# Kernel optimization log

Hardware: AMD Instinct MI355X
Metric: run time of the kernel (lower is better)

Reference implementation:

```python
import jax, jax.numpy as jnp
import numpy as np

SIZE = 896   # hidden_size
HALF = 448   # hidden_size // 2
BINS = 256   # 2 ** (bits / 2)
B, T = 32, 1024


def _scale(x):
    # [0, BINS-1] ints -> [-1, 1] floats
    return x.astype(jnp.float32) / ((BINS - 1) / 2.0) - 1.0


def _reorder(w):
    # torch GRU layout (r, u, e) each split coarse/fine ->
    # (coarse_r, coarse_u, coarse_e, fine_r, fine_u, fine_e)
    cr, fr, cu, fu, ce, fe = jnp.split(w, 6, axis=0)
    return jnp.concatenate([cr, cu, ce, fr, fu, fe], axis=0)


def setup_inputs():
    key = jax.random.key(0)
    ks = jax.random.split(key, 14)
    s = 0.05
    return {
        'conditional': jax.random.normal(ks[0], (B, 3 * SIZE, T), jnp.float32) * s,
        'w_coarse_in': jax.random.normal(ks[1], (3 * HALF, 2), jnp.float32) * s,
        'w_fine_in': jax.random.normal(ks[2], (3 * HALF, 3), jnp.float32) * s,
        'w_hh': jax.random.normal(ks[3], (3 * SIZE, SIZE), jnp.float32) * s,
        'b_ih': jax.random.normal(ks[4], (3 * SIZE,), jnp.float32) * s,
        'b_hh': jax.random.normal(ks[5], (3 * SIZE,), jnp.float32) * s,
        'wc1': jax.random.normal(ks[6], (HALF, HALF), jnp.float32) * s,
        'bc1': jax.random.normal(ks[7], (HALF,), jnp.float32) * s,
        'wc2': jax.random.normal(ks[8], (BINS, HALF), jnp.float32) * s,
        'bc2': jax.random.normal(ks[9], (BINS,), jnp.float32) * s,
        'wf1': jax.random.normal(ks[10], (HALF, HALF), jnp.float32) * s,
        'bf1': jax.random.normal(ks[11], (HALF,), jnp.float32) * s,
        'wf2': jax.random.normal(ks[12], (BINS, HALF), jnp.float32) * s,
        'bf2': jax.random.normal(ks[13], (BINS,), jnp.float32) * s,
    }


def _gru_softmax_step(hid, ip, hp, W1, b1, W2, b2):
    # hid: [HALF, B]; ip, hp: [3*HALF, B]
    ru = jax.nn.sigmoid(hp[:2 * HALF] + ip[:2 * HALF])
    r, u = ru[:HALF], ru[HALF:]
    e = jnp.tanh(r * hp[2 * HALF:] + ip[2 * HALF:])
    hid = u * hid + (1.0 - u) * e
    h = jax.nn.relu(hid.T @ W1.T + b1)          # [B, HALF]
    logits = h @ W2.T + b2                       # [B, BINS]
    sample = jnp.argmax(logits, axis=1).astype(jnp.int32)  # argmax=True path
    return hid, sample


def reference(conditional, w_coarse_in, w_fine_in, w_hh, b_ih, b_hh,
              wc1, bc1, wc2, bc2, wf1, bf1, wf2, bf2):
    batch, _, sig_len = conditional.shape
    # [B, 3*SIZE, T] -> [B, T, 3, SIZE], add input bias, split coarse/fine halves
    cond = conditional.transpose(0, 2, 1).reshape(batch, sig_len, 3, SIZE)
    g = cond + b_ih.reshape(3, SIZE)
    # reshape keeps gate order (r, u, e) concatenated along last dim
    bias_c = g[..., :HALF].reshape(batch, sig_len, 3 * HALF).transpose(1, 2, 0)  # [T, 3H, B]
    bias_f = g[..., HALF:].reshape(batch, sig_len, 3 * HALF).transpose(1, 2, 0)

    w_hh_r = _reorder(w_hh)                 # [3*SIZE, SIZE]
    b_hh_r = _reorder(b_hh[:, None])        # [3*SIZE, 1]

    def step(carry, xs):
        coarse, fine, c_hid, f_hid = carry
        bc, bf = xs
        hidden = jnp.concatenate([c_hid, f_hid], axis=0)        # [SIZE, B]
        hp = w_hh_r @ hidden + b_hh_r                            # [3*SIZE, B]
        hp_c, hp_f = hp[:3 * HALF], hp[3 * HALF:]
        cin = jnp.stack([_scale(coarse), _scale(fine)], axis=1)  # [B, 2]
        c_hid, new_coarse = _gru_softmax_step(
            c_hid, w_coarse_in @ cin.T + bc, hp_c, wc1, bc1, wc2, bc2)
        fin = jnp.stack([_scale(coarse), _scale(fine), _scale(new_coarse)], axis=1)  # [B, 3]
        f_hid, new_fine = _gru_softmax_step(
            f_hid, w_fine_in @ fin.T + bf, hp_f, wf1, bf1, wf2, bf2)
        return (new_coarse, new_fine, c_hid, f_hid), (new_coarse, new_fine)

    init = (jnp.full((batch,), BINS // 2, jnp.int32),   # go coarse sample
            jnp.zeros((batch,), jnp.int32),              # go fine sample
            jnp.zeros((HALF, batch), jnp.float32),
            jnp.zeros((HALF, batch), jnp.float32))
    carry, (oc, of) = jax.lax.scan(step, init, (bias_c, bias_f))
    final_hidden = jnp.concatenate([carry[2], carry[3]], axis=0)  # [SIZE, B]
    return oc.T, of.T, final_hidden
```

## Files before the change

kernel.cpp:

```cpp
#include <hip/hip_runtime.h>
#include <math.h>


#define HALFN  448
#define SIZEN  896
#define RTOT   2688
#define NB     32
#define TSTEPS 1024
#define NWG    224
#define NTHR   512
#define CONDSTR (RTOT * TSTEPS)

#define OFF_HID0  0
#define OFF_HID1  28672
#define OFF_H1GC  57344
#define OFF_H1GF  71680
#define OFF_NCP   86016
#define OFF_NFP   86080
#define OFF_CTR   86144
#define OFF_FLAGS 86400

typedef unsigned long long u64t;

__device__ __forceinline__ int orig_row(int r) {
  int c = r / HALFN, o = r - c * HALFN;
  int oc = (c < 3) ? (2 * c) : (2 * (c - 3) + 1);
  return oc * HALFN + o;
}
__device__ __forceinline__ float sigm(float x) { return 1.0f / (1.0f + expf(-x)); }

__device__ __forceinline__ float gload(const float* p) {
  return __hip_atomic_load(const_cast<float*>(p), __ATOMIC_RELAXED, __HIP_MEMORY_SCOPE_AGENT);
}
__device__ __forceinline__ void gstore(float* p, float v) {
  __hip_atomic_store(p, v, __ATOMIC_RELAXED, __HIP_MEMORY_SCOPE_AGENT);
}
__device__ __forceinline__ u64t gload64(const u64t* p) {
  return __hip_atomic_load(const_cast<u64t*>(p), __ATOMIC_RELAXED, __HIP_MEMORY_SCOPE_AGENT);
}
__device__ __forceinline__ void gstore64(u64t* p, u64t v) {
  __hip_atomic_store(p, v, __ATOMIC_RELAXED, __HIP_MEMORY_SCOPE_AGENT);
}
__device__ __forceinline__ void gmax64(u64t* p, u64t v) {
  __hip_atomic_fetch_max(p, v, __ATOMIC_RELAXED, __HIP_MEMORY_SCOPE_AGENT);
}
__device__ __forceinline__ unsigned ctrload(const unsigned* p) {
  return __hip_atomic_load(const_cast<unsigned*>(p), __ATOMIC_RELAXED, __HIP_MEMORY_SCOPE_AGENT);
}
__device__ __forceinline__ unsigned f2ord(float f) {
  unsigned u = __float_as_uint(f);
  return (u & 0x80000000u) ? ~u : (u | 0x80000000u);
}

struct __align__(16) SM {
  float whh[12][SIZEN];
  float wc1l[2][HALFN];
  float wf1l[2][HALFN];
  float wc2l[8][HALFN];
  float wf2l[8][HALFN];
  float red[8][12][32];
  float condw[12][16][33];
  float hps[6][32];
  float hpfl[6][32];
  float chid[2][32];
  float fhid[2][32];
  float scvo[32];
  float sfvo[32];
  float sncn[32];
  float logit8[8][32];
  float wcil[2][3][2];
  float wfil[2][3][3];
  float bihl[12];
  float bhh_l[12];
  int   pflag;
};

__device__ __forceinline__ void gridbar(unsigned* flags, unsigned ep, int& dead) {
  asm volatile("s_waitcnt vmcnt(0)" ::: "memory");
  __syncthreads();
  if (threadIdx.x == 0)
    __hip_atomic_store(&flags[blockIdx.x], ep, __ATOMIC_RELAXED, __HIP_MEMORY_SCOPE_AGENT);
  if (!dead) {
    int iters = 0;
    for (;;) {
      int ok = 1;
      if (threadIdx.x < NWG) {
        unsigned v = __hip_atomic_load(&flags[threadIdx.x], __ATOMIC_RELAXED, __HIP_MEMORY_SCOPE_AGENT);
        ok = (v >= ep) ? 1 : 0;
      }
      if (__syncthreads_and(ok)) break;
      if (++iters > (1 << 20)) { dead = 1; break; }
      __builtin_amdgcn_s_sleep(1);
    }
  } else {
    __syncthreads();
  }
}

__device__ __forceinline__ void pollctr(unsigned* ctr, unsigned target, int* pf, int& dead) {
  if (!dead) {
    int it = 0;
    for (;;) {
      if (threadIdx.x == 0) *pf = (ctrload(ctr) >= target) ? 1 : 0;
      __syncthreads();
      int f = *pf;
      __syncthreads();
      if (f) break;
      if (++it > (1 << 20)) { dead = 1; break; }
      __builtin_amdgcn_s_sleep(1);
    }
  } else {
    __syncthreads(); __syncthreads();
  }
}

extern "C" __global__ void wavernn_init(float* ws) {
  int i = blockIdx.x * blockDim.x + threadIdx.x;
  int st = gridDim.x * blockDim.x;
  for (int k = i; k < 2 * SIZEN * NB; k += st) ws[k] = 0.0f;
  if (i < 64) ((u64t*)(ws + OFF_NCP))[i] = 0ull;
  if (i < 2) ((unsigned*)(ws + OFF_CTR))[i] = 0u;
  if (i < 256) ((unsigned*)(ws + OFF_FLAGS))[i] = 0u;
}

extern "C" __global__ void __launch_bounds__(NTHR)
wavernn_persist(const float* __restrict__ cond,
                const float* __restrict__ wci, const float* __restrict__ wfi,
                const float* __restrict__ whh, const float* __restrict__ bih,
                const float* __restrict__ bhh,
                const float* __restrict__ wc1, const float* __restrict__ bc1,
                const float* __restrict__ wc2, const float* __restrict__ bc2,
                const float* __restrict__ wf1, const float* __restrict__ bf1,
                const float* __restrict__ wf2, const float* __restrict__ bf2,
                float* __restrict__ out, float* ws) {
  __shared__ SM sm;

  float* hid0 = ws + OFF_HID0;
  float* hid1 = ws + OFF_HID1;
  float* h1gc = ws + OFF_H1GC;
  float* h1gf = ws + OFF_H1GF;
  u64t*  ncp  = (u64t*)(ws + OFF_NCP);
  u64t*  nfp  = (u64t*)(ws + OFF_NFP);
  unsigned* ctr = (unsigned*)(ws + OFF_CTR);
  unsigned* flags = (unsigned*)(ws + OFF_FLAGS);

  const int w = blockIdx.x, tid = threadIdx.x;
  const int b = tid & 31, ks = tid >> 5;
  const bool isHead = (w < NB);
  unsigned ep = 0;
  int dead = 0;

#pragma unroll
  for (int rr = 0; rr < 12; rr++) {
    int R = (rr >> 1) * HALFN + 2 * w + (rr & 1);
    const float* src = whh + (size_t)orig_row(R) * SIZEN;
    for (int k = tid * 4; k < SIZEN; k += NTHR * 4)
      *(float4*)&sm.whh[rr][k] = *(const float4*)&src[k];
  }
  if (tid < 12) sm.bhh_l[tid] = bhh[orig_row((tid >> 1) * HALFN + 2 * w + (tid & 1))];
  for (int k = tid * 4; k < HALFN; k += NTHR * 4) {
    *(float4*)&sm.wc1l[0][k] = *(const float4*)&wc1[(size_t)(2 * w) * HALFN + k];
    *(float4*)&sm.wc1l[1][k] = *(const float4*)&wc1[(size_t)(2 * w + 1) * HALFN + k];
    *(float4*)&sm.wf1l[0][k] = *(const float4*)&wf1[(size_t)(2 * w) * HALFN + k];
    *(float4*)&sm.wf1l[1][k] = *(const float4*)&wf1[(size_t)(2 * w + 1) * HALFN + k];
  }
  if (isHead) {
#pragma unroll
    for (int rr = 0; rr < 8; rr++) {
      for (int k = tid * 4; k < HALFN; k += NTHR * 4) {
        *(float4*)&sm.wc2l[rr][k] = *(const float4*)&wc2[(size_t)(w * 8 + rr) * HALFN + k];
        *(float4*)&sm.wf2l[rr][k] = *(const float4*)&wf2[(size_t)(w * 8 + rr) * HALFN + k];
      }
    }
  }
  if (tid < 12) {
    int rk = tid;
    int R = ((rk >= 6) ? HALFN : 0) + ((rk % 6) >> 1) * SIZEN + 2 * w + (rk & 1);
    sm.bihl[rk] = bih[R];
  }
  if (tid < 2) {
    int j = 2 * w + tid;
#pragma unroll
    for (int g = 0; g < 3; g++) {
      sm.wcil[tid][g][0] = wci[(g * HALFN + j) * 2 + 0];
      sm.wcil[tid][g][1] = wci[(g * HALFN + j) * 2 + 1];
      sm.wfil[tid][g][0] = wfi[(g * HALFN + j) * 3 + 0];
      sm.wfil[tid][g][1] = wfi[(g * HALFN + j) * 3 + 1];
      sm.wfil[tid][g][2] = wfi[(g * HALFN + j) * 3 + 2];
    }
  }
  if (tid < 64) { sm.chid[tid >> 5][tid & 31] = 0.0f; sm.fhid[tid >> 5][tid & 31] = 0.0f; }
  if (tid < 32) { sm.scvo[tid] = 128.0f * (2.0f / 255.0f) - 1.0f; sm.sfvo[tid] = -1.0f; }
  __syncthreads();

  for (int t = 0; t < TSTEPS; ++t) {
    const float* hprev = (t & 1) ? hid0 : hid1;
    float*       hcur  = (t & 1) ? hid1 : hid0;
    const int tt = t & 15;

    {
      if (tt == 0) {
        for (int idx = tid; idx < 1536; idx += NTHR) {
          int rk = idx >> 7, rem = idx & 127;
          int bb = rem >> 2, part = rem & 3;
          int R = ((rk >= 6) ? HALFN : 0) + ((rk % 6) >> 1) * SIZEN + 2 * w + (rk & 1);
          float4 v = *(const float4*)&cond[(size_t)bb * CONDSTR + (size_t)R * TSTEPS + t + part * 4];
          sm.condw[rk][part * 4 + 0][bb] = v.x;
          sm.condw[rk][part * 4 + 1][bb] = v.y;
          sm.condw[rk][part * 4 + 2][bb] = v.z;
          sm.condw[rk][part * 4 + 3][bb] = v.w;
        }
      }

      float acc[12];
#pragma unroll
      for (int rr = 0; rr < 12; rr++) acc[rr] = 0.0f;
      const int k0 = ks * 56;
      const float* hcol = hprev + b;
#pragma unroll 2
      for (int k = k0; k < k0 + 56; k += 4) {
        float h0 = gload(&hcol[(k + 0) * 32]), h1v = gload(&hcol[(k + 1) * 32]);
        float h2 = gload(&hcol[(k + 2) * 32]), h3  = gload(&hcol[(k + 3) * 32]);
#pragma unroll
        for (int rr = 0; rr < 12; rr++) {
          const float4 wv = *(const float4*)&sm.whh[rr][k];
          acc[rr] = fmaf(wv.x, h0, fmaf(wv.y, h1v, fmaf(wv.z, h2, fmaf(wv.w, h3, acc[rr]))));
        }
      }
#pragma unroll
      for (int rr = 0; rr < 12; rr++) acc[rr] += __shfl_xor(acc[rr], 32);
      __syncthreads();
      if ((tid & 32) == 0) {
        int slot = ks >> 1;
#pragma unroll
        for (int rr = 0; rr < 12; rr++) sm.red[slot][rr][b] = acc[rr];
      }
      __syncthreads();
      if (tid < 384) {
        int rr = tid >> 5, bb = tid & 31;
        float s = sm.bhh_l[rr];
#pragma unroll
        for (int kk = 0; kk < 8; kk++) s += sm.red[kk][rr][bb];
        if (rr < 6) sm.hps[rr][bb] = s;
        else        sm.hpfl[rr - 6][bb] = s;
      }
      if (t > 0) {
        pollctr(&ctr[1], 32u * (unsigned)t, &sm.pflag, dead);
        if (tid < 32) {
          u64t p = gload64(&nfp[tid]);
          unsigned nf = 0xFFFFFFFFu - (unsigned)(p & 0xFFFFFFFFull);
          sm.sfvo[tid] = (float)nf * (2.0f / 255.0f) - 1.0f;
          if (isHead && tid == w) out[32768 + (size_t)w * TSTEPS + (t - 1)] = (float)nf;
        }
      }
      __syncthreads();
      if (tid < 64) {
        int q = tid >> 5, bb = tid & 31;
        float sc = sm.scvo[bb], sf = sm.sfvo[bb];
        float ipr = sm.wcil[q][0][0] * sc + sm.wcil[q][0][1] * sf + sm.condw[0 + q][tt][bb] + sm.bihl[0 + q];
        float ipu = sm.wcil[q][1][0] * sc + sm.wcil[q][1][1] * sf + sm.condw[2 + q][tt][bb] + sm.bihl[2 + q];
        float ipe = sm.wcil[q][2][0] * sc + sm.wcil[q][2][1] * sf + sm.condw[4 + q][tt][bb] + sm.bihl[4 + q];
        float r = sigm(sm.hps[0 + q][bb] + ipr);
        float u = sigm(sm.hps[2 + q][bb] + ipu);
        float e = tanhf(fmaf(r, sm.hps[4 + q][bb], ipe));
        float hnew = u * sm.chid[q][bb] + (1.0f - u) * e;
        sm.chid[q][bb] = hnew;
        gstore(&hcur[(size_t)(2 * w + q) * 32 + bb], hnew);
      }
    }
    gridbar(flags, ++ep, dead);

    {
      const int k0 = ks * 28;
      float a0 = 0.0f, a1 = 0.0f;
      const float* hcc = hcur + b;
#pragma unroll
      for (int k = k0; k < k0 + 28; k += 4) {
        float h0 = gload(&hcc[(k + 0) * 32]), h1v = gload(&hcc[(k + 1) * 32]);
        float h2 = gload(&hcc[(k + 2) * 32]), h3  = gload(&hcc[(k + 3) * 32]);
        float4 v0 = *(const float4*)&sm.wc1l[0][k];
        a0 = fmaf(v0.x, h0, fmaf(v0.y, h1v, fmaf(v0.z, h2, fmaf(v0.w, h3, a0))));
        float4 v1 = *(const float4*)&sm.wc1l[1][k];
        a1 = fmaf(v1.x, h0, fmaf(v1.y, h1v, fmaf(v1.z, h2, fmaf(v1.w, h3, a1))));
      }
      a0 += __shfl_xor(a0, 32); a1 += __shfl_xor(a1, 32);
      __syncthreads();
      if ((tid & 32) == 0) { sm.red[ks >> 1][0][b] = a0; sm.red[ks >> 1][1][b] = a1; }
      if (isHead && tid == 256) gstore64(&ncp[w], 0ull);
      __syncthreads();
      if (tid < 64) {
        int rr = tid >> 5, bb = tid & 31;
        float s = bc1[2 * w + rr];
#pragma unroll
        for (int kk = 0; kk < 8; kk++) s += sm.red[kk][rr][bb];
        gstore(&h1gc[(size_t)(2 * w + rr) * 32 + bb], fmaxf(s, 0.0f));
      }
    }
    gridbar(flags, ++ep, dead);

    if (isHead) {
      const int k0 = ks * 28;
      float acc[8];
#pragma unroll
      for (int rr = 0; rr < 8; rr++) acc[rr] = 0.0f;
      const float* hh = h1gc + b;
#pragma unroll
      for (int k = k0; k < k0 + 28; k += 4) {
        float h0 = gload(&hh[(k + 0) * 32]), h1v = gload(&hh[(k + 1) * 32]);
        float h2 = gload(&hh[(k + 2) * 32]), h3  = gload(&hh[(k + 3) * 32]);
#pragma unroll
        for (int rr = 0; rr < 8; rr++) {
          const float4 wv = *(const float4*)&sm.wc2l[rr][k];
          acc[rr] = fmaf(wv.x, h0, fmaf(wv.y, h1v, fmaf(wv.z, h2, fmaf(wv.w, h3, acc[rr]))));
        }
      }
#pragma unroll
      for (int rr = 0; rr < 8; rr++) acc[rr] += __shfl_xor(acc[rr], 32);
      __syncthreads();
      if ((tid & 32) == 0) {
        int slot = ks >> 1;
#pragma unroll
        for (int rr = 0; rr < 8; rr++) sm.red[slot][rr][b] = acc[rr];
      }
      __syncthreads();
      if (tid < 256) {
        int rr = tid >> 5, bb = tid & 31;
        float s = bc2[w * 8 + rr];
#pragma unroll
        for (int kk = 0; kk < 8; kk++) s += sm.red[kk][rr][bb];
        sm.logit8[rr][bb] = s;
      }
      __syncthreads();
      if (tid < 32) {
        float bv = sm.logit8[0][tid]; int bi = 0;
#pragma unroll
        for (int rr = 1; rr < 8; rr++) {
          float x = sm.logit8[rr][tid];
          if (x > bv) { bv = x; bi = rr; }
        }
        u64t pack = ((u64t)f2ord(bv) << 32) | (u64t)(0xFFFFFFFFu - (unsigned)(w * 8 + bi));
        gmax64(&ncp[tid], pack);
      }
      asm volatile("s_waitcnt vmcnt(0)" ::: "memory");
      __syncthreads();
      if (tid == 0) __hip_atomic_fetch_add(&ctr[0], 1u, __ATOMIC_RELAXED, __HIP_MEMORY_SCOPE_AGENT);
    }
    pollctr(&ctr[0], 32u * (unsigned)(t + 1), &sm.pflag, dead);

    {
      if (tid < 32) {
        u64t p = gload64(&ncp[tid]);
        unsigned nc = 0xFFFFFFFFu - (unsigned)(p & 0xFFFFFFFFull);
        sm.sncn[tid] = (float)nc * (2.0f / 255.0f) - 1.0f;
        if (isHead && tid == w) out[(size_t)w * TSTEPS + t] = (float)nc;
      }
      __syncthreads();
      if (tid < 64) {
        int q = tid >> 5, bb = tid & 31;
        float sc = sm.scvo[bb], sf = sm.sfvo[bb], snc = sm.sncn[bb];
        float ipr = sm.wfil[q][0][0] * sc + sm.wfil[q][0][1] * sf + sm.wfil[q][0][2] * snc
                  + sm.condw[6 + q][tt][bb] + sm.bihl[6 + q];
        float ipu = sm.wfil[q][1][0] * sc + sm.wfil[q][1][1] * sf + sm.wfil[q][1][2] * snc
                  + sm.condw[8 + q][tt][bb] + sm.bihl[8 + q];
        float ipe = sm.wfil[q][2][0] * sc + sm.wfil[q][2][1] * sf + sm.wfil[q][2][2] * snc
                  + sm.condw[10 + q][tt][bb] + sm.bihl[10 + q];
        float r = sigm(sm.hpfl[0 + q][bb] + ipr);
        float u = sigm(sm.hpfl[2 + q][bb] + ipu);
        float e = tanhf(fmaf(r, sm.hpfl[4 + q][bb], ipe));
        float hnew = u * sm.fhid[q][bb] + (1.0f - u) * e;
        sm.fhid[q][bb] = hnew;
        gstore(&hcur[(size_t)(HALFN + 2 * w + q) * 32 + bb], hnew);
      }
      __syncthreads();
      if (tid < 32) sm.scvo[tid] = sm.sncn[tid];
    }
    gridbar(flags, ++ep, dead);

    {
      const int k0 = ks * 28;
      float a0 = 0.0f, a1 = 0.0f;
      const float* hff = hcur + HALFN * 32 + b;
#pragma unroll
      for (int k = k0; k < k0 + 28; k += 4) {
        float h0 = gload(&hff[(k + 0) * 32]), h1v = gload(&hff[(k + 1) * 32]);
        float h2 = gload(&hff[(k + 2) * 32]), h3  = gload(&hff[(k + 3) * 32]);
        float4 v0 = *(const float4*)&sm.wf1l[0][k];
        a0 = fmaf(v0.x, h0, fmaf(v0.y, h1v, fmaf(v0.z, h2, fmaf(v0.w, h3, a0))));
        float4 v1 = *(const float4*)&sm.wf1l[1][k];
        a1 = fmaf(v1.x, h0, fmaf(v1.y, h1v, fmaf(v1.z, h2, fmaf(v1.w, h3, a1))));
      }
      a0 += __shfl_xor(a0, 32); a1 += __shfl_xor(a1, 32);
      __syncthreads();
      if ((tid & 32) == 0) { sm.red[ks >> 1][0][b] = a0; sm.red[ks >> 1][1][b] = a1; }
      if (isHead && tid == 256) gstore64(&nfp[w], 0ull);
      __syncthreads();
      if (tid < 64) {
        int rr = tid >> 5, bb = tid & 31;
        float s = bf1[2 * w + rr];
#pragma unroll
        for (int kk = 0; kk < 8; kk++) s += sm.red[kk][rr][bb];
        gstore(&h1gf[(size_t)(2 * w + rr) * 32 + bb], fmaxf(s, 0.0f));
      }
    }
    gridbar(flags, ++ep, dead);

    if (isHead) {
      const int k0 = ks * 28;
      float acc[8];
#pragma unroll
      for (int rr = 0; rr < 8; rr++) acc[rr] = 0.0f;
      const float* hh = h1gf + b;
#pragma unroll
      for (int k = k0; k < k0 + 28; k += 4) {
        float h0 = gload(&hh[(k + 0) * 32]), h1v = gload(&hh[(k + 1) * 32]);
        float h2 = gload(&hh[(k + 2) * 32]), h3  = gload(&hh[(k + 3) * 32]);
#pragma unroll
        for (int rr = 0; rr < 8; rr++) {
          const float4 wv = *(const float4*)&sm.wf2l[rr][k];
          acc[rr] = fmaf(wv.x, h0, fmaf(wv.y, h1v, fmaf(wv.z, h2, fmaf(wv.w, h3, acc[rr]))));
        }
      }
#pragma unroll
      for (int rr = 0; rr < 8; rr++) acc[rr] += __shfl_xor(acc[rr], 32);
      __syncthreads();
      if ((tid & 32) == 0) {
        int slot = ks >> 1;
#pragma unroll
        for (int rr = 0; rr < 8; rr++) sm.red[slot][rr][b] = acc[rr];
      }
      __syncthreads();
      if (tid < 256) {
        int rr = tid >> 5, bb = tid & 31;
        float s = bf2[w * 8 + rr];
#pragma unroll
        for (int kk = 0; kk < 8; kk++) s += sm.red[kk][rr][bb];
        sm.logit8[rr][bb] = s;
      }
      __syncthreads();
      if (tid < 32) {
        float bv = sm.logit8[0][tid]; int bi = 0;
#pragma unroll
        for (int rr = 1; rr < 8; rr++) {
          float x = sm.logit8[rr][tid];
          if (x > bv) { bv = x; bi = rr; }
        }
        u64t pack = ((u64t)f2ord(bv) << 32) | (u64t)(0xFFFFFFFFu - (unsigned)(w * 8 + bi));
        gmax64(&nfp[tid], pack);
      }
      asm volatile("s_waitcnt vmcnt(0)" ::: "memory");
      __syncthreads();
      if (tid == 0) __hip_atomic_fetch_add(&ctr[1], 1u, __ATOMIC_RELAXED, __HIP_MEMORY_SCOPE_AGENT);
    }
  }

  pollctr(&ctr[1], 32u * (unsigned)TSTEPS, &sm.pflag, dead);
  if (tid < 32 && isHead && tid == w) {
    u64t p = gload64(&nfp[tid]);
    unsigned nf = 0xFFFFFFFFu - (unsigned)(p & 0xFFFFFFFFull);
    out[32768 + (size_t)w * TSTEPS + (TSTEPS - 1)] = (float)nf;
  }
  if (tid < 64) {
    int q = tid >> 5, bb = tid & 31;
    out[65536 + (size_t)(2 * w + q) * 32 + bb]         = sm.chid[q][bb];
    out[65536 + (size_t)(HALFN + 2 * w + q) * 32 + bb] = sm.fhid[q][bb];
  }
}

extern "C" void kernel_launch(void* const* d_in, const int* in_sizes, int n_in,
                              void* d_out, int out_size, void* d_ws, size_t ws_size,
                              hipStream_t stream) {
  const float* cond = (const float*)d_in[0];
  const float* wci  = (const float*)d_in[1];
  const float* wfi  = (const float*)d_in[2];
  const float* whh  = (const float*)d_in[3];
  const float* bih  = (const float*)d_in[4];
  const float* bhh  = (const float*)d_in[5];
  const float* wc1  = (const float*)d_in[6];
  const float* bc1  = (const float*)d_in[7];
  const float* wc2  = (const float*)d_in[8];
  const float* bc2  = (const float*)d_in[9];
  const float* wf1  = (const float*)d_in[10];
  const float* bf1  = (const float*)d_in[11];
  const float* wf2  = (const float*)d_in[12];
  const float* bf2  = (const float*)d_in[13];
  float* out = (float*)d_out;
  float* ws  = (float*)d_ws;

  hipLaunchKernelGGL(wavernn_init, dim3(64), dim3(256), 0, stream, ws);
  hipLaunchKernelGGL(wavernn_persist, dim3(NWG), dim3(NTHR), 0, stream,
                     cond, wci, wfi, whh, bih, bhh,
                     wc1, bc1, wc2, bc2, wf1, bf1, wf2, bf2, out, ws);
}
```

Baseline: 31.06 ms.

## Spread second FC layer and argmax across all workgroups with per-batch counters

The second output layer (448->256) and argmax were done by only 32 head workgroups while the other 192 idled; now all 224 workgroups each own a 9-10 row slice of the output and a 4-batch group, staging the relu hidden vector in LDS with a transposed global layout. Completion is signalled by per-batch counters, each expecting 28 arrivals, instead of one global counter, and the poll checks all of them with a single block-wide AND instead of two barriers per iteration. This shortens the serial critical path per timestep but adds more atomics on ncp/nfp and more LDS traffic. The clearing of ncp/nfp is also swapped between the two phases.

```diff
diff --git a/kernel.cpp b/kernel.cpp
--- a/kernel.cpp
+++ b/kernel.cpp
@@ -10,15 +10,18 @@
 #define NWG    224
 #define NTHR   512
 #define CONDSTR (RTOT * TSTEPS)
+#define RBN    28
+#define FANIN  28
 
 #define OFF_HID0  0
 #define OFF_HID1  28672
-#define OFF_H1GC  57344
-#define OFF_H1GF  71680
+#define OFF_H1TC  57344
+#define OFF_H1TF  71680
 #define OFF_NCP   86016
 #define OFF_NFP   86080
-#define OFF_CTR   86144
-#define OFF_FLAGS 86400
+#define OFF_DCTRC 86144
+#define OFF_DCTRF 86176
+#define OFF_FLAGS 86208
 
 typedef unsigned long long u64t;
 
@@ -56,23 +59,24 @@
   float whh[12][SIZEN];
   float wc1l[2][HALFN];
   float wf1l[2][HALFN];
-  float wc2l[8][HALFN];
-  float wf2l[8][HALFN];
+  float wc2l[10][HALFN];
+  float wf2l[10][HALFN];
   float red[8][12][32];
   float condw[12][16][33];
+  float h1c4[4][HALFN];
+  float fcr[4][16][8];
+  float flog[4][16];
   float hps[6][32];
   float hpfl[6][32];
   float chid[2][32];
   float fhid[2][32];
-  float scvo[32];
-  float sfvo[32];
-  float sncn[32];
-  float logit8[8][32];
+  float scvo[32], sfvo[32], sncn[32];
+  float ncraw[32], nfraw[32];
   float wcil[2][3][2];
   float wfil[2][3][3];
   float bihl[12];
   float bhh_l[12];
-  int   pflag;
+  float bc2l[10], bf2l[10];
 };
 
 __device__ __forceinline__ void gridbar(unsigned* flags, unsigned ep, int& dead) {
@@ -97,20 +101,19 @@
   }
 }
 
-__device__ __forceinline__ void pollctr(unsigned* ctr, unsigned target, int* pf, int& dead) {
+__device__ __forceinline__ void pollmany(unsigned* arr, int n, unsigned target, int& dead) {
   if (!dead) {
     int it = 0;
     for (;;) {
-      if (threadIdx.x == 0) *pf = (ctrload(ctr) >= target) ? 1 : 0;
-      __syncthreads();
-      int f = *pf;
-      __syncthreads();
-      if (f) break;
+      int ok = 1;
+      if ((int)threadIdx.x < n)
+        ok = (ctrload(&arr[threadIdx.x]) >= target) ? 1 : 0;
+      if (__syncthreads_and(ok)) break;
       if (++it > (1 << 20)) { dead = 1; break; }
       __builtin_amdgcn_s_sleep(1);
     }
   } else {
-    __syncthreads(); __syncthreads();
+    __syncthreads();
   }
 }
 
@@ -119,7 +122,7 @@
   int st = gridDim.x * blockDim.x;
   for (int k = i; k < 2 * SIZEN * NB; k += st) ws[k] = 0.0f;
   if (i < 64) ((u64t*)(ws + OFF_NCP))[i] = 0ull;
-  if (i < 2) ((unsigned*)(ws + OFF_CTR))[i] = 0u;
+  if (i < 64) ((unsigned*)(ws + OFF_DCTRC))[i] = 0u;
   if (i < 256) ((unsigned*)(ws + OFF_FLAGS))[i] = 0u;
 }
 
@@ -137,16 +140,19 @@
 
   float* hid0 = ws + OFF_HID0;
   float* hid1 = ws + OFF_HID1;
-  float* h1gc = ws + OFF_H1GC;
-  float* h1gf = ws + OFF_H1GF;
+  float* h1tc = ws + OFF_H1TC;
+  float* h1tf = ws + OFF_H1TF;
   u64t*  ncp  = (u64t*)(ws + OFF_NCP);
   u64t*  nfp  = (u64t*)(ws + OFF_NFP);
-  unsigned* ctr = (unsigned*)(ws + OFF_CTR);
+  unsigned* dctrc = (unsigned*)(ws + OFF_DCTRC);
+  unsigned* dctrf = (unsigned*)(ws + OFF_DCTRF);
   unsigned* flags = (unsigned*)(ws + OFF_FLAGS);
 
   const int w = blockIdx.x, tid = threadIdx.x;
   const int b = tid & 31, ks = tid >> 5;
-  const bool isHead = (w < NB);
+  const int rb = w >> 3, bg = w & 7;
+  const int fc2start = (rb < 4) ? rb * 10 : 40 + (rb - 4) * 9;
+  const int fc2len   = (rb < 4) ? 10 : 9;
   unsigned ep = 0;
   int dead = 0;
 
@@ -164,15 +170,13 @@
     *(float4*)&sm.wf1l[0][k] = *(const float4*)&wf1[(size_t)(2 * w) * HALFN + k];
     *(float4*)&sm.wf1l[1][k] = *(const float4*)&wf1[(size_t)(2 * w + 1) * HALFN + k];
   }
-  if (isHead) {
-#pragma unroll
-    for (int rr = 0; rr < 8; rr++) {
-      for (int k = tid * 4; k < HALFN; k += NTHR * 4) {
-        *(float4*)&sm.wc2l[rr][k] = *(const float4*)&wc2[(size_t)(w * 8 + rr) * HALFN + k];
-        *(float4*)&sm.wf2l[rr][k] = *(const float4*)&wf2[(size_t)(w * 8 + rr) * HALFN + k];
-      }
-    }
-  }
+  for (int rr = 0; rr < fc2len; rr++) {
+    for (int k = tid * 4; k < HALFN; k += NTHR * 4) {
+      *(float4*)&sm.wc2l[rr][k] = *(const float4*)&wc2[(size_t)(fc2start + rr) * HALFN + k];
+      *(float4*)&sm.wf2l[rr][k] = *(const float4*)&wf2[(size_t)(fc2start + rr) * HALFN + k];
+    }
+  }
+  if (tid < fc2len) { sm.bc2l[tid] = bc2[fc2start + tid]; sm.bf2l[tid] = bf2[fc2start + tid]; }
   if (tid < 12) {
     int rk = tid;
     int R = ((rk >= 6) ? HALFN : 0) + ((rk % 6) >> 1) * SIZEN + 2 * w + (rk & 1);
@@ -245,15 +249,17 @@
         else        sm.hpfl[rr - 6][bb] = s;
       }
       if (t > 0) {
-        pollctr(&ctr[1], 32u * (unsigned)t, &sm.pflag, dead);
+        pollmany(dctrf, 32, FANIN * (unsigned)t, dead);
         if (tid < 32) {
           u64t p = gload64(&nfp[tid]);
           unsigned nf = 0xFFFFFFFFu - (unsigned)(p & 0xFFFFFFFFull);
           sm.sfvo[tid] = (float)nf * (2.0f / 255.0f) - 1.0f;
-          if (isHead && tid == w) out[32768 + (size_t)w * TSTEPS + (t - 1)] = (float)nf;
-        }
-      }
-      __syncthreads();
+          sm.nfraw[tid] = (float)nf;
+        }
+      }
+      __syncthreads();
+      if (t > 0 && w < 32 && tid == 64)
+        out[32768 + (size_t)w * TSTEPS + (t - 1)] = sm.nfraw[w];
       if (tid < 64) {
         int q = tid >> 5, bb = tid & 31;
         float sc = sm.scvo[bb], sf = sm.sfvo[bb];
@@ -286,75 +292,74 @@
       a0 += __shfl_xor(a0, 32); a1 += __shfl_xor(a1, 32);
       __syncthreads();
       if ((tid & 32) == 0) { sm.red[ks >> 1][0][b] = a0; sm.red[ks >> 1][1][b] = a1; }
-      if (isHead && tid == 256) gstore64(&ncp[w], 0ull);
+      if (w < 32 && tid == 256) gstore64(&nfp[w], 0ull);
       __syncthreads();
       if (tid < 64) {
         int rr = tid >> 5, bb = tid & 31;
         float s = bc1[2 * w + rr];
 #pragma unroll
         for (int kk = 0; kk < 8; kk++) s += sm.red[kk][rr][bb];
-        gstore(&h1gc[(size_t)(2 * w + rr) * 32 + bb], fmaxf(s, 0.0f));
+        gstore(&h1tc[(size_t)bb * HALFN + 2 * w + rr], fmaxf(s, 0.0f));
       }
     }
     gridbar(flags, ++ep, dead);
 
-    if (isHead) {
-      const int k0 = ks * 28;
-      float acc[8];
-#pragma unroll
-      for (int rr = 0; rr < 8; rr++) acc[rr] = 0.0f;
-      const float* hh = h1gc + b;
-#pragma unroll
-      for (int k = k0; k < k0 + 28; k += 4) {
-        float h0 = gload(&hh[(k + 0) * 32]), h1v = gload(&hh[(k + 1) * 32]);
-        float h2 = gload(&hh[(k + 2) * 32]), h3  = gload(&hh[(k + 3) * 32]);
-#pragma unroll
-        for (int rr = 0; rr < 8; rr++) {
-          const float4 wv = *(const float4*)&sm.wc2l[rr][k];
-          acc[rr] = fmaf(wv.x, h0, fmaf(wv.y, h1v, fmaf(wv.z, h2, fmaf(wv.w, h3, acc[rr]))));
-        }
-      }
-#pragma unroll
-      for (int rr = 0; rr < 8; rr++) acc[rr] += __shfl_xor(acc[rr], 32);
-      __syncthreads();
-      if ((tid & 32) == 0) {
-        int slot = ks >> 1;
-#pragma unroll
-        for (int rr = 0; rr < 8; rr++) sm.red[slot][rr][b] = acc[rr];
-      }
-      __syncthreads();
-      if (tid < 256) {
-        int rr = tid >> 5, bb = tid & 31;
-        float s = bc2[w * 8 + rr];
-#pragma unroll
-        for (int kk = 0; kk < 8; kk++) s += sm.red[kk][rr][bb];
-        sm.logit8[rr][bb] = s;
-      }
-      __syncthreads();
-      if (tid < 32) {
-        float bv = sm.logit8[0][tid]; int bi = 0;
-#pragma unroll
-        for (int rr = 1; rr < 8; rr++) {
-          float x = sm.logit8[rr][tid];
-          if (x > bv) { bv = x; bi = rr; }
-        }
-        u64t pack = ((u64t)f2ord(bv) << 32) | (u64t)(0xFFFFFFFFu - (unsigned)(w * 8 + bi));
-        gmax64(&ncp[tid], pack);
-      }
-      asm volatile("s_waitcnt vmcnt(0)" ::: "memory");
-      __syncthreads();
-      if (tid == 0) __hip_atomic_fetch_add(&ctr[0], 1u, __ATOMIC_RELAXED, __HIP_MEMORY_SCOPE_AGENT);
-    }
-    pollctr(&ctr[0], 32u * (unsigned)(t + 1), &sm.pflag, dead);
+    {
+#pragma unroll
+      for (int bq = 0; bq < 4; bq++)
+        if (tid < HALFN) sm.h1c4[bq][tid] = gload(&h1tc[(size_t)(4 * bg + bq) * HALFN + tid]);
+      __syncthreads();
+      {
+        int bq = tid >> 7, rl = (tid >> 3) & 15, kss = tid & 7;
+        if (rl < fc2len) {
+          const float* wrow = sm.wc2l[rl];
+          const float* hcol = sm.h1c4[bq];
+          float a = 0.0f;
+          int kk0 = kss * 56;
+#pragma unroll
+          for (int k = kk0; k < kk0 + 56; k += 4) {
+            float4 wv = *(const float4*)&wrow[k];
+            float4 hv = *(const float4*)&hcol[k];
+            a = fmaf(wv.x, hv.x, fmaf(wv.y, hv.y, fmaf(wv.z, hv.z, fmaf(wv.w, hv.w, a))));
+          }
+          sm.fcr[bq][rl][kss] = a;
+        }
+      }
+      __syncthreads();
+      if (tid < 64) {
+        int bq = tid >> 4, rl = tid & 15;
+        if (rl < fc2len) {
+          float s = sm.bc2l[rl];
+#pragma unroll
+          for (int q = 0; q < 8; q++) s += sm.fcr[bq][rl][q];
+          sm.flog[bq][rl] = s;
+        }
+      }
+      __syncthreads();
+      if (tid < 4) {
+        int bq = tid;
+        float bv = sm.flog[bq][0]; int bi = 0;
+        for (int rl = 1; rl < fc2len; rl++) {
+          float x = sm.flog[bq][rl];
+          if (x > bv) { bv = x; bi = rl; }
+        }
+        u64t pack = ((u64t)f2ord(bv) << 32) | (u64t)(0xFFFFFFFFu - (unsigned)(fc2start + bi));
+        gmax64(&ncp[4 * bg + bq], pack);
+        asm volatile("s_waitcnt vmcnt(0)" ::: "memory");
+        __hip_atomic_fetch_add(&dctrc[4 * bg + bq], 1u, __ATOMIC_RELAXED, __HIP_MEMORY_SCOPE_AGENT);
+      }
+    }
+    pollmany(dctrc, 32, FANIN * (unsigned)(t + 1), dead);
 
     {
       if (tid < 32) {
         u64t p = gload64(&ncp[tid]);
         unsigned nc = 0xFFFFFFFFu - (unsigned)(p & 0xFFFFFFFFull);
         sm.sncn[tid] = (float)nc * (2.0f / 255.0f) - 1.0f;
-        if (isHead && tid == w) out[(size_t)w * TSTEPS + t] = (float)nc;
-      }
-      __syncthreads();
+        sm.ncraw[tid] = (float)nc;
+      }
+      __syncthreads();
+      if (w < 32 && tid == 64) out[(size_t)w * TSTEPS + t] = sm.ncraw[w];
       if (tid < 64) {
         int q = tid >> 5, bb = tid & 31;
         float sc = sm.scvo[bb], sf = sm.sfvo[bb], snc = sm.sncn[bb];
@@ -392,70 +397,68 @@
       a0 += __shfl_xor(a0, 32); a1 += __shfl_xor(a1, 32);
       __syncthreads();
       if ((tid & 32) == 0) { sm.red[ks >> 1][0][b] = a0; sm.red[ks >> 1][1][b] = a1; }
-      if (isHead && tid == 256) gstore64(&nfp[w], 0ull);
+      if (w < 32 && tid == 256) gstore64(&ncp[w], 0ull);
       __syncthreads();
       if (tid < 64) {
         int rr = tid >> 5, bb = tid & 31;
         float s = bf1[2 * w + rr];
 #pragma unroll
         for (int kk = 0; kk < 8; kk++) s += sm.red[kk][rr][bb];
-        gstore(&h1gf[(size_t)(2 * w + rr) * 32 + bb], fmaxf(s, 0.0f));
+        gstore(&h1tf[(size_t)bb * HALFN + 2 * w + rr], fmaxf(s, 0.0f));
       }
     }
     gridbar(flags, ++ep, dead);
 
-    if (isHead) {
-      const int k0 = ks * 28;
-      float acc[8];
-#pragma unroll
-      for (int rr = 0; rr < 8; rr++) acc[rr] = 0.0f;
-      const float* hh = h1gf + b;
-#pragma unroll
-      for (int k = k0; k < k0 + 28; k += 4) {
-        float h0 = gload(&hh[(k + 0) * 32]), h1v = gload(&hh[(k + 1) * 32]);
-        float h2 = gload(&hh[(k + 2) * 32]), h3  = gload(&hh[(k + 3) * 32]);
-#pragma unroll
-        for (int rr = 0; rr < 8; rr++) {
-          const float4 wv = *(const float4*)&sm.wf2l[rr][k];
-          acc[rr] = fmaf(wv.x, h0, fmaf(wv.y, h1v, fmaf(wv.z, h2, fmaf(wv.w, h3, acc[rr]))));
-        }
-      }
-#pragma unroll
-      for (int rr = 0; rr < 8; rr++) acc[rr] += __shfl_xor(acc[rr], 32);
-      __syncthreads();
-      if ((tid & 32) == 0) {
-        int slot = ks >> 1;
-#pragma unroll
-        for (int rr = 0; rr < 8; rr++) sm.red[slot][rr][b] = acc[rr];
-      }
-      __syncthreads();
-      if (tid < 256) {
-        int rr = tid >> 5, bb = tid & 31;
-        float s = bf2[w * 8 + rr];
-#pragma unroll
-        for (int kk = 0; kk < 8; kk++) s += sm.red[kk][rr][bb];
-        sm.logit8[rr][bb] = s;
-      }
-      __syncthreads();
-      if (tid < 32) {
-        float bv = sm.logit8[0][tid]; int bi = 0;
-#pragma unroll
-        for (int rr = 1; rr < 8; rr++) {
-          float x = sm.logit8[rr][tid];
-          if (x > bv) { bv = x; bi = rr; }
-        }
-        u64t pack = ((u64t)f2ord(bv) << 32) | (u64t)(0xFFFFFFFFu - (unsigned)(w * 8 + bi));
-        gmax64(&nfp[tid], pack);
-      }
-      asm volatile("s_waitcnt vmcnt(0)" ::: "memory");
-      __syncthreads();
-      if (tid == 0) __hip_atomic_fetch_add(&ctr[1], 1u, __ATOMIC_RELAXED, __HIP_MEMORY_SCOPE_AGENT);
-    }
-  }
-
-  pollctr(&ctr[1], 32u * (unsigned)TSTEPS, &sm.pflag, dead);
-  if (tid < 32 && isHead && tid == w) {
-    u64t p = gload64(&nfp[tid]);
+    {
+#pragma unroll
+      for (int bq = 0; bq < 4; bq++)
+        if (tid < HALFN) sm.h1c4[bq][tid] = gload(&h1tf[(size_t)(4 * bg + bq) * HALFN + tid]);
+      __syncthreads();
+      {
+        int bq = tid >> 7, rl = (tid >> 3) & 15, kss = tid & 7;
+        if (rl < fc2len) {
+          const float* wrow = sm.wf2l[rl];
+          const float* hcol = sm.h1c4[bq];
+          float a = 0.0f;
+          int kk0 = kss * 56;
+#pragma unroll
+          for (int k = kk0; k < kk0 + 56; k += 4) {
+            float4 wv = *(const float4*)&wrow[k];
+            float4 hv = *(const float4*)&hcol[k];
+            a = fmaf(wv.x, hv.x, fmaf(wv.y, hv.y, fmaf(wv.z, hv.z, fmaf(wv.w, hv.w, a))));
+          }
+          sm.fcr[bq][rl][kss] = a;
+        }
+      }
+      __syncthreads();
+      if (tid < 64) {
+        int bq = tid >> 4, rl = tid & 15;
+        if (rl < fc2len) {
+          float s = sm.bf2l[rl];
+#pragma unroll
+          for (int q = 0; q < 8; q++) s += sm.fcr[bq][rl][q];
+          sm.flog[bq][rl] = s;
+        }
+      }
+      __syncthreads();
+      if (tid < 4) {
+        int bq = tid;
+        float bv = sm.flog[bq][0]; int bi = 0;
+        for (int rl = 1; rl < fc2len; rl++) {
+          float x = sm.flog[bq][rl];
+          if (x > bv) { bv = x; bi = rl; }
+        }
+        u64t pack = ((u64t)f2ord(bv) << 32) | (u64t)(0xFFFFFFFFu - (unsigned)(fc2start + bi));
+        gmax64(&nfp[4 * bg + bq], pack);
+        asm volatile("s_waitcnt vmcnt(0)" ::: "memory");
+        __hip_atomic_fetch_add(&dctrf[4 * bg + bq], 1u, __ATOMIC_RELAXED, __HIP_MEMORY_SCOPE_AGENT);
+      }
+    }
+  }
+
+  pollmany(dctrf, 32, FANIN * (unsigned)TSTEPS, dead);
+  if (w < 32 && tid == 0) {
+    u64t p = gload64(&nfp[w]);
     unsigned nf = 0xFFFFFFFFu - (unsigned)(p & 0xFFFFFFFFull);
     out[32768 + (size_t)w * TSTEPS + (TSTEPS - 1)] = (float)nf;
   }
```

Measured after the change: 31.50 ms. No clear change (+1.4%).
